# Kernel optimization log

Measured on AMD Instinct MI355X. Metric: run time of the kernel, lower is better.

The kernel has to match this reference:

```python
import jax, jax.numpy as jnp
import numpy as np
import math

N_HEAD = 16

def setup_inputs() -> dict:
    key = jax.random.key(0)
    k1, k2, k3, k4, k5 = jax.random.split(key, 5)
    B, T, C = 8, 1024, 1024
    scale = 0.02
    return {
        "x": jax.random.normal(k1, (B, T, C), dtype=jnp.float32),
        "w_attn": jax.random.normal(k2, (C, 3 * C), dtype=jnp.float32) * scale,
        "b_attn": jax.random.normal(k3, (3 * C,), dtype=jnp.float32) * scale,
        "w_proj": jax.random.normal(k4, (C, C), dtype=jnp.float32) * scale,
        "b_proj": jax.random.normal(k5, (C,), dtype=jnp.float32) * scale,
    }

def reference(x, w_attn, b_attn, w_proj, b_proj):
    B, T, C = x.shape
    H = N_HEAD
    hd = C // H
    # QKV projection: [B,T,3C]
    qkv = jnp.einsum("btc,cd->btd", x, w_attn) + b_attn
    q, k, v = jnp.split(qkv, 3, axis=-1)
    # [B,T,C] -> [B,H,T,hd]
    def heads(t):
        return t.reshape(B, T, H, hd).transpose(0, 2, 1, 3)
    q, k, v = heads(q), heads(k), heads(v)
    # scaled QK^T: [B,H,T,T]
    att = jnp.einsum("bhqd,bhkd->bhqk", q, k) * (1.0 / math.sqrt(hd))
    # causal mask (tril of block_size cropped to T)
    causal = jnp.tril(jnp.ones((T, T), dtype=bool))
    att = jnp.where(causal, att, jnp.float32(-jnp.inf))
    att = jax.nn.softmax(att, axis=-1)
    # attention-weighted values: [B,H,T,hd] -> [B,T,C]
    y = jnp.einsum("bhqk,bhkd->bhqd", att, v)
    y = y.transpose(0, 2, 1, 3).reshape(B, T, C)
    # output projection
    return jnp.einsum("btc,cd->btd", y, w_proj) + b_proj
```

## Files before the change

### kernel.cpp

```cpp
#include <hip/hip_runtime.h>

typedef __bf16 bf16x8 __attribute__((ext_vector_type(8)));
typedef float f32x4 __attribute__((ext_vector_type(4)));
typedef unsigned short u16;
typedef unsigned int u32;
typedef unsigned long long u64;

__device__ __forceinline__ u16 f2bf(float f) {
  u32 u = __builtin_bit_cast(u32, f);
  u32 r = (u + 0x7FFFu + ((u >> 16) & 1u)) >> 16;
  return (u16)r;
}

__device__ __forceinline__ void gload_lds16(const u16* g, u16* l) {
  __builtin_amdgcn_global_load_lds(
      (const __attribute__((address_space(1))) u32*)g,
      (__attribute__((address_space(3))) u32*)l, 16, 0, 0);
}

__global__ void cast_x_kernel(const float* __restrict__ in, u16* __restrict__ out, int n4) {
  int i = blockIdx.x * blockDim.x + threadIdx.x;
  if (i >= n4) return;
  float4 v = ((const float4*)in)[i];
  uint2 o;
  o.x = (u32)f2bf(v.x) | ((u32)f2bf(v.y) << 16);
  o.y = (u32)f2bf(v.z) | ((u32)f2bf(v.w) << 16);
  ((uint2*)out)[i] = o;
}

__global__ void transpose_cast_kernel(const float* __restrict__ in, u16* __restrict__ out,
                                      int K, int N) {
  __shared__ float tile[32][33];
  int n0 = blockIdx.x * 32, k0 = blockIdx.y * 32;
  int tx = threadIdx.x & 31, ty = threadIdx.x >> 5;
#pragma unroll
  for (int i = 0; i < 32; i += 8)
    tile[ty + i][tx] = in[(size_t)(k0 + ty + i) * N + n0 + tx];
  __syncthreads();
#pragma unroll
  for (int i = 0; i < 32; i += 8)
    out[(size_t)(n0 + ty + i) * K + k0 + tx] = f2bf(tile[tx][ty + i]);
}

template <int MODE>
__global__ __launch_bounds__(256, 3) void gemm_bf16(
    const u16* __restrict__ A, const u16* __restrict__ Bt,
    const float* __restrict__ bias, u16* __restrict__ out_q,
    float* __restrict__ out_f, int M, int N, int K) {
  __shared__ alignas(16) u16 As[128 * 64];
  __shared__ alignas(16) u16 Bs[128 * 64];
  const int tiles_n = N >> 7;
  const int bid0 = blockIdx.x;
  const int cpx = (int)gridDim.x >> 3;
  const int swz = (bid0 & 7) * cpx + (bid0 >> 3);
  const int tm = swz / tiles_n;
  const int tn = swz % tiles_n;
  const int tid = threadIdx.x;
  const int wave = tid >> 6, lane = tid & 63;
  const int wr = (wave >> 1) * 64, wc = (wave & 1) * 64;
  const int lr = lane & 15, lg = lane >> 4;

  f32x4 acc[4][4] = {};
  const size_t a_base = (size_t)(tm * 128) * K;
  const size_t b_base = (size_t)(tn * 128) * K;

  for (int k0 = 0; k0 < K; k0 += 64) {
#pragma unroll
    for (int i = 0; i < 4; ++i) {
      int c = i * 256 + tid;
      int row = c >> 3, ch = c & 7;
      int sw = (ch ^ (row & 7)) * 8;
      gload_lds16(A + a_base + (size_t)row * K + k0 + sw, &As[c * 8]);
      gload_lds16(Bt + b_base + (size_t)row * K + k0 + sw, &Bs[c * 8]);
    }
    __syncthreads();
    bf16x8 af[4][2], bfr[4][2];
#pragma unroll
    for (int m = 0; m < 4; ++m) {
      int row = wr + m * 16 + lr;
#pragma unroll
      for (int kk = 0; kk < 2; ++kk)
        af[m][kk] = *(const bf16x8*)&As[(row * 64 + kk * 32 + lg * 8) ^ ((row & 7) << 3)];
    }
#pragma unroll
    for (int n = 0; n < 4; ++n) {
      int row = wc + n * 16 + lr;
#pragma unroll
      for (int kk = 0; kk < 2; ++kk)
        bfr[n][kk] = *(const bf16x8*)&Bs[(row * 64 + kk * 32 + lg * 8) ^ ((row & 7) << 3)];
    }
#pragma unroll
    for (int m = 0; m < 4; ++m)
#pragma unroll
      for (int n = 0; n < 4; ++n) {
        if constexpr (MODE == 0) {
          acc[m][n] = __builtin_amdgcn_mfma_f32_16x16x32_bf16(bfr[n][0], af[m][0], acc[m][n], 0, 0, 0);
          acc[m][n] = __builtin_amdgcn_mfma_f32_16x16x32_bf16(bfr[n][1], af[m][1], acc[m][n], 0, 0, 0);
        } else {
          acc[m][n] = __builtin_amdgcn_mfma_f32_16x16x32_bf16(af[m][0], bfr[n][0], acc[m][n], 0, 0, 0);
          acc[m][n] = __builtin_amdgcn_mfma_f32_16x16x32_bf16(af[m][1], bfr[n][1], acc[m][n], 0, 0, 0);
        }
      }
    __syncthreads();
  }

  if constexpr (MODE == 0) {
    const int tok0 = tm * 128 + wr;
    const int col0 = tn * 128 + wc;
#pragma unroll
    for (int n = 0; n < 4; ++n) {
      int ncol = col0 + n * 16 + lg * 4;
      float4 bv = *(const float4*)&bias[ncol];
      int which = ncol >> 10, c = ncol & 1023;
      int h = c >> 6, d = c & 63;
#pragma unroll
      for (int m = 0; m < 4; ++m) {
        int tok = tok0 + m * 16 + lr;
        int b = tok >> 10, t = tok & 1023;
        union { u16 s[4]; uint2 v; } pk;
        pk.s[0] = f2bf(acc[m][n][0] + bv.x);
        pk.s[1] = f2bf(acc[m][n][1] + bv.y);
        pk.s[2] = f2bf(acc[m][n][2] + bv.z);
        pk.s[3] = f2bf(acc[m][n][3] + bv.w);
        *(uint2*)&out_q[(size_t)which * 8388608 + ((((size_t)b * 16 + h) * 1024 + t) << 6) + d] = pk.v;
      }
    }
  } else if constexpr (MODE == 2) {
    const int tok0 = tm * 128 + wr;
    const int col0 = tn * 128 + wc;
#pragma unroll
    for (int n = 0; n < 4; ++n) {
      int ncol = col0 + n * 16 + lr;
      float bv = bias[ncol];
      int h = ncol >> 6, d = ncol & 63;
#pragma unroll
      for (int m = 0; m < 4; ++m) {
        int t0 = tok0 + m * 16 + lg * 4;
        int b = t0 >> 10, t = t0 & 1023;
        union { u16 s[4]; uint2 v; } pk;
        pk.s[0] = f2bf(acc[m][n][0] + bv);
        pk.s[1] = f2bf(acc[m][n][1] + bv);
        pk.s[2] = f2bf(acc[m][n][2] + bv);
        pk.s[3] = f2bf(acc[m][n][3] + bv);
        *(uint2*)&out_q[(((size_t)b * 16 + h) * 64 + d) * 1024 + t] = pk.v;
      }
    }
  } else {
    const int row0 = tm * 128 + wr;
    const int col0 = tn * 128 + wc;
#pragma unroll
    for (int n = 0; n < 4; ++n) {
      int col = col0 + n * 16 + lr;
      float bv = bias[col];
#pragma unroll
      for (int m = 0; m < 4; ++m)
#pragma unroll
        for (int r = 0; r < 4; ++r) {
          int mrow = row0 + m * 16 + lg * 4 + r;
          out_f[(size_t)mrow * N + col] = acc[m][n][r] + bv;
        }
    }
  }
}

__global__ __launch_bounds__(256, 2) void attn_kernel(
    const u16* __restrict__ Qb, const u16* __restrict__ Kb,
    const u16* __restrict__ Vb, u16* __restrict__ yb) {
  __shared__ alignas(16) u16 Ks[128 * 64];
  __shared__ alignas(16) u16 Vt[64 * 128];
  __shared__ alignas(16) u16 Pl[4][32 * 64];

  const int bid = blockIdx.x;
  const int xcd = bid & 7, j = bid >> 3;
  const int bh = ((j >> 2) << 3) + xcd;
  const int pr = j & 3;
  const size_t hb = (size_t)bh * 65536;
  const int tid = threadIdx.x, w = tid >> 6, lane = tid & 63;
  const int lr = lane & 15, lg = lane >> 4;
  const int b = bh >> 4, h = bh & 15;
  const float C2 = 0.18033688011112042f;

  for (int pass = 0; pass < 2; ++pass) {
    const int qt = pass ? (7 - pr) : pr;
    const int q0 = qt * 128 + w * 32;

    bf16x8 qf[2][2];
#pragma unroll
    for (int mi = 0; mi < 2; ++mi)
#pragma unroll
      for (int ks = 0; ks < 2; ++ks)
        qf[mi][ks] = *(const bf16x8*)&Qb[hb + (size_t)(q0 + mi * 16 + lr) * 64 + ks * 32 + lg * 8];

    float m_run[2] = {-1e30f, -1e30f}, l_run[2] = {0.f, 0.f};
    f32x4 o[2][4] = {};

    const int nkt = qt + 1;
    for (int kt = 0; kt < nkt; ++kt) {
#pragma unroll
      for (int i = 0; i < 4; ++i) {
        int c = i * 256 + tid;
        int row = c >> 3, ch = c & 7;
        gload_lds16(Kb + hb + (size_t)(kt * 128 + row) * 64 + ((ch ^ (row & 7)) * 8), &Ks[c * 8]);
      }
#pragma unroll
      for (int i = 0; i < 4; ++i) {
        int c = i * 256 + tid;
        int row = c >> 4, ch = c & 15;
        gload_lds16(Vb + hb + (size_t)row * 1024 + kt * 128 + ((ch ^ (row & 15)) * 8), &Vt[c * 8]);
      }
      __syncthreads();

      f32x4 s[8][2] = {};
      __builtin_amdgcn_s_setprio(1);
#pragma unroll
      for (int ni = 0; ni < 8; ++ni) {
        int krow = ni * 16 + lr;
        bf16x8 kf0 = *(const bf16x8*)&Ks[(krow * 64 + lg * 8) ^ ((krow & 7) << 3)];
        bf16x8 kf1 = *(const bf16x8*)&Ks[(krow * 64 + 32 + lg * 8) ^ ((krow & 7) << 3)];
#pragma unroll
        for (int mi = 0; mi < 2; ++mi) {
          s[ni][mi] = __builtin_amdgcn_mfma_f32_16x16x32_bf16(kf0, qf[mi][0], s[ni][mi], 0, 0, 0);
          s[ni][mi] = __builtin_amdgcn_mfma_f32_16x16x32_bf16(kf1, qf[mi][1], s[ni][mi], 0, 0, 0);
        }
      }
      __builtin_amdgcn_s_setprio(0);

      const bool need_mask = (kt == qt);
      float alpha_l[2];
#pragma unroll
      for (int mi = 0; mi < 2; ++mi) {
        if (need_mask) {
#pragma unroll
          for (int ni = 0; ni < 8; ++ni)
#pragma unroll
            for (int r = 0; r < 4; ++r) {
              int ka = kt * 128 + ni * 16 + lg * 4 + r;
              int qa = q0 + mi * 16 + lr;
              if (ka > qa) s[ni][mi][r] = -1e30f;
            }
        }
        float pm[8];
#pragma unroll
        for (int ni = 0; ni < 8; ++ni)
          pm[ni] = fmaxf(fmaxf(s[ni][mi][0], s[ni][mi][1]), fmaxf(s[ni][mi][2], s[ni][mi][3]));
        float v = fmaxf(fmaxf(fmaxf(pm[0], pm[1]), fmaxf(pm[2], pm[3])),
                        fmaxf(fmaxf(pm[4], pm[5]), fmaxf(pm[6], pm[7])));
        v = fmaxf(v, __shfl_xor(v, 16));
        v = fmaxf(v, __shfl_xor(v, 32));
        float mn = fmaxf(m_run[mi], v);
        float mc = mn * C2;
        float al = __builtin_amdgcn_exp2f(m_run[mi] * C2 - mc);
        m_run[mi] = mn;
        float ps[8];
#pragma unroll
        for (int ni = 0; ni < 8; ++ni) {
#pragma unroll
          for (int r = 0; r < 4; ++r)
            s[ni][mi][r] = __builtin_amdgcn_exp2f(fmaf(s[ni][mi][r], C2, -mc));
          ps[ni] = (s[ni][mi][0] + s[ni][mi][1]) + (s[ni][mi][2] + s[ni][mi][3]);
        }
        float rs = ((ps[0] + ps[1]) + (ps[2] + ps[3])) + ((ps[4] + ps[5]) + (ps[6] + ps[7]));
        rs += __shfl_xor(rs, 16);
        rs += __shfl_xor(rs, 32);
        l_run[mi] = l_run[mi] * al + rs;
        alpha_l[mi] = al;
      }
#pragma unroll
      for (int mi = 0; mi < 2; ++mi) {
        f32x4 av;
#pragma unroll
        for (int r = 0; r < 4; ++r) av[r] = __shfl(alpha_l[mi], lg * 4 + r);
#pragma unroll
        for (int nd = 0; nd < 4; ++nd)
#pragma unroll
          for (int r = 0; r < 4; ++r) o[mi][nd][r] *= av[r];
      }
#pragma unroll
      for (int hh = 0; hh < 2; ++hh) {
#pragma unroll
        for (int mi = 0; mi < 2; ++mi) {
          int qrow = mi * 16 + lr;
          int sw = (qrow & 7) << 3;
#pragma unroll
          for (int nq = 0; nq < 4; ++nq) {
            int ni = hh * 4 + nq;
            u32 plo, phi;
            asm("v_cvt_pk_bf16_f32 %0, %1, %2" : "=v"(plo) : "v"(s[ni][mi][0]), "v"(s[ni][mi][1]));
            asm("v_cvt_pk_bf16_f32 %0, %1, %2" : "=v"(phi) : "v"(s[ni][mi][2]), "v"(s[ni][mi][3]));
            u64 pv = (u64)plo | ((u64)phi << 32);
            int e = (qrow * 64 + nq * 16 + lg * 4) ^ sw;
            *(u64*)&Pl[w][e] = pv;
          }
        }
        asm volatile("s_waitcnt lgkmcnt(0)" ::: "memory");
        __builtin_amdgcn_s_setprio(1);
#pragma unroll
        for (int kh = 0; kh < 2; ++kh) {
          int ks = hh * 2 + kh;
          bf16x8 pf[2];
#pragma unroll
          for (int mi = 0; mi < 2; ++mi) {
            int prow = mi * 16 + lr;
            pf[mi] = *(const bf16x8*)&Pl[w][(prow * 64 + kh * 32 + lg * 8) ^ ((prow & 7) << 3)];
          }
#pragma unroll
          for (int nd = 0; nd < 4; ++nd) {
            int vrow = nd * 16 + lr;
            bf16x8 vf = *(const bf16x8*)&Vt[(vrow * 128 + ks * 32 + lg * 8) ^ ((vrow & 15) << 3)];
#pragma unroll
            for (int mi = 0; mi < 2; ++mi)
              o[mi][nd] = __builtin_amdgcn_mfma_f32_16x16x32_bf16(pf[mi], vf, o[mi][nd], 0, 0, 0);
          }
        }
        __builtin_amdgcn_s_setprio(0);
      }
      __syncthreads();
    }

#pragma unroll
    for (int mi = 0; mi < 2; ++mi) {
      f32x4 inv;
#pragma unroll
      for (int r = 0; r < 4; ++r) inv[r] = 1.f / __shfl(l_run[mi], lg * 4 + r);
#pragma unroll
      for (int nd = 0; nd < 4; ++nd)
#pragma unroll
        for (int r = 0; r < 4; ++r) {
          int t = q0 + mi * 16 + lg * 4 + r;
          int c = h * 64 + nd * 16 + lr;
          yb[((size_t)b * 1024 + t) * 1024 + c] = f2bf(o[mi][nd][r] * inv[r]);
        }
    }
    __syncthreads();
  }
}

extern "C" void kernel_launch(void* const* d_in, const int* in_sizes, int n_in,
                              void* d_out, int out_size, void* d_ws, size_t ws_size,
                              hipStream_t stream) {
  const float* x = (const float*)d_in[0];
  const float* w_attn = (const float*)d_in[1];
  const float* b_attn = (const float*)d_in[2];
  const float* w_proj = (const float*)d_in[3];
  const float* b_proj = (const float*)d_in[4];
  float* out = (float*)d_out;

  u16* ws = (u16*)d_ws;
  u16* xb = ws;
  u16* watT = xb + 8388608;
  u16* wpT = watT + 3145728;
  u16* Qb = wpT + 1048576;
  u16* Vt = Qb + 2 * 8388608;
  u16* yb = xb;

  cast_x_kernel<<<8192, 256, 0, stream>>>(x, xb, 2097152);
  {
    dim3 g(96, 32);
    transpose_cast_kernel<<<g, 256, 0, stream>>>(w_attn, watT, 1024, 3072);
  }
  {
    dim3 g(32, 32);
    transpose_cast_kernel<<<g, 256, 0, stream>>>(w_proj, wpT, 1024, 1024);
  }
  gemm_bf16<0><<<64 * 16, 256, 0, stream>>>(xb, watT, b_attn, Qb, nullptr, 8192, 2048, 1024);
  gemm_bf16<2><<<64 * 8, 256, 0, stream>>>(xb, watT + (size_t)2048 * 1024, b_attn + 2048, Vt,
                                           nullptr, 8192, 1024, 1024);
  attn_kernel<<<512, 256, 0, stream>>>(Qb, Qb + 8388608, Vt, yb);
  gemm_bf16<1><<<64 * 8, 256, 0, stream>>>(yb, wpT, b_proj, nullptr, out, 8192, 1024, 1024);
}
```

Measured before the change: 156.6 us.

## Double-buffer K/V tiles in attention kernel to overlap loads with compute

Splits the K and V shared-memory tiles into two buffers and issues the global-to-LDS loads for the next key tile before computing on the current one. Explicit vmcnt waits and raw barriers replace the full __syncthreads so the prefetch stays in flight during the MFMA work. This doubles the K/V LDS footprint (about 64KB plus the P buffers per block), which may reduce occupancy below the two blocks per CU the launch bounds request.

```diff
diff --git a/kernel.cpp b/kernel.cpp
--- a/kernel.cpp
+++ b/kernel.cpp
@@ -166,8 +166,8 @@
 __global__ __launch_bounds__(256, 2) void attn_kernel(
     const u16* __restrict__ Qb, const u16* __restrict__ Kb,
     const u16* __restrict__ Vb, u16* __restrict__ yb) {
-  __shared__ alignas(16) u16 Ks[128 * 64];
-  __shared__ alignas(16) u16 Vt[64 * 128];
+  __shared__ alignas(16) u16 Ks[2][128 * 64];
+  __shared__ alignas(16) u16 Vt[2][64 * 128];
   __shared__ alignas(16) u16 Pl[4][32 * 64];
 
   const int bid = blockIdx.x;
@@ -180,6 +180,21 @@
   const int b = bh >> 4, h = bh & 15;
   const float C2 = 0.18033688011112042f;
 
+  auto stageKV = [&](int kt, u16* ksb, u16* vtb) {
+#pragma unroll
+    for (int i = 0; i < 4; ++i) {
+      int c = i * 256 + tid;
+      int row = c >> 3, ch = c & 7;
+      gload_lds16(Kb + hb + (size_t)(kt * 128 + row) * 64 + ((ch ^ (row & 7)) * 8), &ksb[c * 8]);
+    }
+#pragma unroll
+    for (int i = 0; i < 4; ++i) {
+      int c = i * 256 + tid;
+      int row = c >> 4, ch = c & 15;
+      gload_lds16(Vb + hb + (size_t)row * 1024 + kt * 128 + ((ch ^ (row & 15)) * 8), &vtb[c * 8]);
+    }
+  };
+
   for (int pass = 0; pass < 2; ++pass) {
     const int qt = pass ? (7 - pr) : pr;
     const int q0 = qt * 128 + w * 32;
@@ -195,28 +210,26 @@
     f32x4 o[2][4] = {};
 
     const int nkt = qt + 1;
+    stageKV(0, Ks[0], Vt[0]);
     for (int kt = 0; kt < nkt; ++kt) {
-#pragma unroll
-      for (int i = 0; i < 4; ++i) {
-        int c = i * 256 + tid;
-        int row = c >> 3, ch = c & 7;
-        gload_lds16(Kb + hb + (size_t)(kt * 128 + row) * 64 + ((ch ^ (row & 7)) * 8), &Ks[c * 8]);
-      }
-#pragma unroll
-      for (int i = 0; i < 4; ++i) {
-        int c = i * 256 + tid;
-        int row = c >> 4, ch = c & 15;
-        gload_lds16(Vb + hb + (size_t)row * 1024 + kt * 128 + ((ch ^ (row & 15)) * 8), &Vt[c * 8]);
-      }
-      __syncthreads();
+      const int cur = kt & 1;
+      if (kt + 1 < nkt) {
+        stageKV(kt + 1, Ks[cur ^ 1], Vt[cur ^ 1]);
+        asm volatile("s_waitcnt vmcnt(8)" ::: "memory");
+      } else {
+        asm volatile("s_waitcnt vmcnt(0)" ::: "memory");
+      }
+      __builtin_amdgcn_s_barrier();
+      const u16* ks_ = Ks[cur];
+      const u16* vt_ = Vt[cur];
 
       f32x4 s[8][2] = {};
       __builtin_amdgcn_s_setprio(1);
 #pragma unroll
       for (int ni = 0; ni < 8; ++ni) {
         int krow = ni * 16 + lr;
-        bf16x8 kf0 = *(const bf16x8*)&Ks[(krow * 64 + lg * 8) ^ ((krow & 7) << 3)];
-        bf16x8 kf1 = *(const bf16x8*)&Ks[(krow * 64 + 32 + lg * 8) ^ ((krow & 7) << 3)];
+        bf16x8 kf0 = *(const bf16x8*)&ks_[(krow * 64 + lg * 8) ^ ((krow & 7) << 3)];
+        bf16x8 kf1 = *(const bf16x8*)&ks_[(krow * 64 + 32 + lg * 8) ^ ((krow & 7) << 3)];
 #pragma unroll
         for (int mi = 0; mi < 2; ++mi) {
           s[ni][mi] = __builtin_amdgcn_mfma_f32_16x16x32_bf16(kf0, qf[mi][0], s[ni][mi], 0, 0, 0);
@@ -296,7 +309,7 @@
         __builtin_amdgcn_s_setprio(1);
 #pragma unroll
         for (int kh = 0; kh < 2; ++kh) {
-          int ks = hh * 2 + kh;
+          int ksl = hh * 2 + kh;
           bf16x8 pf[2];
 #pragma unroll
           for (int mi = 0; mi < 2; ++mi) {
@@ -306,7 +319,7 @@
 #pragma unroll
           for (int nd = 0; nd < 4; ++nd) {
             int vrow = nd * 16 + lr;
-            bf16x8 vf = *(const bf16x8*)&Vt[(vrow * 128 + ks * 32 + lg * 8) ^ ((vrow & 15) << 3)];
+            bf16x8 vf = *(const bf16x8*)&vt_[(vrow * 128 + ksl * 32 + lg * 8) ^ ((vrow & 15) << 3)];
 #pragma unroll
             for (int mi = 0; mi < 2; ++mi)
               o[mi][nd] = __builtin_amdgcn_mfma_f32_16x16x32_bf16(pf[mi], vf, o[mi][nd], 0, 0, 0);
@@ -314,7 +327,8 @@
         }
         __builtin_amdgcn_s_setprio(0);
       }
-      __syncthreads();
+      asm volatile("s_waitcnt lgkmcnt(0)" ::: "memory");
+      __builtin_amdgcn_s_barrier();
     }
 
 #pragma unroll
```

After: 163.3 us. +4.3%, slower.
